# Kernel optimization log

Hardware: AMD Instinct MI355X
Metric: run time of the kernel (lower is better)

## Reference

```python
import jax, jax.numpy as jnp
import numpy as np
import math


def gen_slopes(n_heads, alibi_bias_max=1.0):
    # matches torch gen_slopes: _n_heads = next pow2, m = arange(1.._n)*max/_n, slopes = 2^-m
    _n = 2 ** math.ceil(math.log2(n_heads))
    m = jnp.arange(1, _n + 1, dtype=jnp.float32) * (alibi_bias_max / _n)
    slopes = 1.0 / jnp.power(2.0, m)
    if _n != n_heads:
        slopes = jnp.concatenate([slopes[1::2], slopes[::2]])[:n_heads]
    return slopes.reshape(1, n_heads, 1, 1)


def build_alibi_bias(n_heads, seq_len, alibi_bias_max=1.0):
    # full=False branch: bias over key positions only, shape [1, H, 1, L]
    pos = jnp.arange(1 - seq_len, 1, dtype=jnp.float32).reshape(1, 1, 1, seq_len)
    return pos * gen_slopes(n_heads, alibi_bias_max)


def setup_inputs() -> dict:
    key = jax.random.key(0)
    kq, kk, kv = jax.random.split(key, 3)
    B, L, H, E = 8, 1024, 8, 64
    return {
        "queries": jax.random.normal(kq, (B, L, H, E), dtype=jnp.float32),
        "keys": jax.random.normal(kk, (B, L, H, E), dtype=jnp.float32),
        "values": jax.random.normal(kv, (B, L, H, E), dtype=jnp.float32),
        "patch_index": -1,
    }


def reference(queries, keys, values, patch_index):
    B, L, H, E = queries.shape
    scale = 1.0 / math.sqrt(E)
    # scores: [B, H, L, L]
    scores = jnp.einsum('blhe,bshe->bhls', queries, keys)
    attn = scale * scores + build_alibi_bias(H, L)  # ALiBi bias, alibi_bias_max=1
    series = jax.nn.softmax(attn, axis=-1)  # dropout is identity in eval mode
    V = jnp.einsum('bhls,bshd->blhd', series, values)
    # patch_index == -1: identity branch, series unchanged
    return (V, series)
```

## Files before the change

### kernel.cpp

```cpp
#include <hip/hip_runtime.h>
#include <hip/hip_bf16.h>


typedef short short8 __attribute__((ext_vector_type(8)));
typedef short short4v __attribute__((ext_vector_type(4)));
typedef float f32x4 __attribute__((ext_vector_type(4)));
typedef unsigned short u16x4 __attribute__((ext_vector_type(4)));

#define B_ 8
#define L_ 1024
#define H_ 8
#define E_ 64
#define RSTRIDE (H_ * E_)
#define QBLK 64
#define CHUNK 128
#define NCH (L_ / CHUNK)
#define CHUNK_USH (CHUNK * E_)

__device__ __forceinline__ unsigned short f2bf(float f) {
  return __builtin_bit_cast(unsigned short, __float2bfloat16(f));
}
__device__ __forceinline__ short8 ldfrag(const float* p) {
  float4 a = *reinterpret_cast<const float4*>(p);
  float4 b = *reinterpret_cast<const float4*>(p + 4);
  return (short8){(short)f2bf(a.x), (short)f2bf(a.y), (short)f2bf(a.z),
                  (short)f2bf(a.w), (short)f2bf(b.x), (short)f2bf(b.y),
                  (short)f2bf(b.z), (short)f2bf(b.w)};
}

__device__ __forceinline__ f32x4 mfma16(short4v a, short4v b, f32x4 c) {
#if __has_builtin(__builtin_amdgcn_mfma_f32_16x16x16bf16_1k)
  return __builtin_amdgcn_mfma_f32_16x16x16bf16_1k(a, b, c, 0, 0, 0);
#else
  asm volatile(
      "s_nop 1\n\t"
      "v_mfma_f32_16x16x16_bf16 %0, %1, %2, %0\n\t"
      "s_nop 2"
      : "+v"(c)
      : "v"(a), "v"(b));
  return c;
#endif
}

__device__ __forceinline__ void gld16(const unsigned short* g,
                                      unsigned short* l) {
  __builtin_amdgcn_global_load_lds(
      (const __attribute__((address_space(1))) unsigned int*)g,
      (__attribute__((address_space(3))) unsigned int*)l, 16, 0, 0);
}

__global__ __launch_bounds__(256, 4) void prep_kv(
    const float* __restrict__ Kg, const float* __restrict__ Vg,
    unsigned short* __restrict__ Kbf, unsigned short* __restrict__ VTbf) {
  __shared__ unsigned short vt[64 * 128];

  const int t = threadIdx.x;
  const int id = blockIdx.x;
  const int bh = id & 63;
  const int sc = id >> 6;
  const int h = bh & 7, b = bh >> 3;
  const int s0 = sc * CHUNK;

  const float* Kb = Kg + ((size_t)b * L_ + s0) * RSTRIDE + h * E_;
  const float* Vb = Vg + ((size_t)b * L_ + s0) * RSTRIDE + h * E_;
  unsigned short* Ko = Kbf + (size_t)(bh * NCH + sc) * CHUNK_USH;
  unsigned short* Vo = VTbf + (size_t)(bh * NCH + sc) * CHUNK_USH;

#pragma unroll
  for (int i = 0; i < 4; ++i) {
    const int j = t + 256 * i;
    const int s = j >> 3;
    const int e8 = (j & 7) ^ (s & 7);
    const float* kp = Kb + (size_t)s * RSTRIDE + 8 * e8;
    float4 a = *reinterpret_cast<const float4*>(kp);
    float4 c = *reinterpret_cast<const float4*>(kp + 4);
    *reinterpret_cast<u16x4*>(&Ko[j * 8]) =
        (u16x4){f2bf(a.x), f2bf(a.y), f2bf(a.z), f2bf(a.w)};
    *reinterpret_cast<u16x4*>(&Ko[j * 8 + 4]) =
        (u16x4){f2bf(c.x), f2bf(c.y), f2bf(c.z), f2bf(c.w)};
  }
  {
    const int e = t & 63, w = t >> 6;
#pragma unroll
    for (int i = 0; i < 8; ++i) {
      const int s4 = 4 * w + 16 * i;
      const float* vp = Vb + (size_t)s4 * RSTRIDE + e;
      u16x4 u = {f2bf(vp[0]), f2bf(vp[RSTRIDE]), f2bf(vp[2 * RSTRIDE]),
                 f2bf(vp[3 * RSTRIDE])};
      *reinterpret_cast<u16x4*>(
          &vt[e * 128 + (((s4 >> 3) ^ (e & 7)) << 3) + (s4 & 7)]) = u;
    }
  }
  __syncthreads();
#pragma unroll
  for (int i = 0; i < 4; ++i) {
    const int j = t + 256 * i;
    u16x4 u0 = *reinterpret_cast<const u16x4*>(&vt[j * 8]);
    u16x4 u1 = *reinterpret_cast<const u16x4*>(&vt[j * 8 + 4]);
    *reinterpret_cast<u16x4*>(&Vo[j * 8]) = u0;
    *reinterpret_cast<u16x4*>(&Vo[j * 8 + 4]) = u1;
  }
}

__global__ __launch_bounds__(256, 4) void alibi_attn(
    const float* __restrict__ Qg, const unsigned short* __restrict__ Kbf,
    const unsigned short* __restrict__ VTbf, float* __restrict__ Vout,
    float* __restrict__ Pout) {
  __shared__ unsigned short sK[CHUNK_USH];
  __shared__ unsigned short sVT[CHUNK_USH];

  const int t = threadIdx.x;
  const int lane = t & 63;
  const int w = t >> 6;
  const int col = lane & 15;
  const int kg = lane >> 4;

  const int id = blockIdx.x;
  const int qb = id >> 6;
  const int bh = id & 63;
  const int h = bh & 7;
  const int b = bh >> 3;
  const int q0 = qb * QBLK;

  const float sc_l2e = 0.125f * 1.44269504f;
  const float sl_l2e = exp2f(-(float)(h + 1) * 0.125f) * 1.44269504f;

  const unsigned short* Kc = Kbf + (size_t)bh * NCH * CHUNK_USH;
  const unsigned short* Vc = VTbf + (size_t)bh * NCH * CHUNK_USH;

  short8 qf0, qf1;
  {
    const float* qp =
        Qg + ((size_t)b * L_ + q0 + 16 * w + col) * RSTRIDE + h * E_ + 8 * kg;
    qf0 = ldfrag(qp);
    qf1 = ldfrag(qp + 32);
  }

  const float kbias0 = sl_l2e * (float)(4 * kg - 1023) - 32.0f;

  float z0 = 0.f, z1 = 0.f, z2 = 0.f, z3 = 0.f;
  for (int c = 0; c < NCH; ++c) {
    {
      const unsigned short* src = Kc + (size_t)c * CHUNK_USH;
#pragma unroll
      for (int i = 0; i < 4; ++i) {
        const int seg = i * 4 + w;
        gld16(src + (size_t)(seg * 64 + lane) * 8, &sK[seg * 512]);
      }
    }
    __syncthreads();
#pragma unroll 4
    for (int kt = 0; kt < 8; ++kt) {
      const int row = 16 * kt + col;
      short8 k0 = *reinterpret_cast<const short8*>(
          &sK[row * 64 + ((kg ^ (row & 7)) << 3)]);
      short8 k1 = *reinterpret_cast<const short8*>(
          &sK[row * 64 + (((kg + 4) ^ (row & 7)) << 3)]);
      f32x4 acc = {0.f, 0.f, 0.f, 0.f};
      acc = __builtin_amdgcn_mfma_f32_16x16x32_bf16(k0, qf0, acc, 0, 0, 0);
      acc = __builtin_amdgcn_mfma_f32_16x16x32_bf16(k1, qf1, acc, 0, 0, 0);
      const float base = fmaf((float)(128 * c + 16 * kt), sl_l2e, kbias0);
      z0 += __builtin_amdgcn_exp2f(fmaf(acc[0], sc_l2e, base));
      z1 += __builtin_amdgcn_exp2f(fmaf(acc[1], sc_l2e, base + sl_l2e));
      z2 += __builtin_amdgcn_exp2f(fmaf(acc[2], sc_l2e, base + 2.f * sl_l2e));
      z3 += __builtin_amdgcn_exp2f(fmaf(acc[3], sc_l2e, base + 3.f * sl_l2e));
    }
    __syncthreads();
  }
  float z = (z0 + z1) + (z2 + z3);
  z += __shfl_xor(z, 16, 64);
  z += __shfl_xor(z, 32, 64);
  const float minv = 1.0f / z;

  f32x4 oacc[4];
#pragma unroll
  for (int et = 0; et < 4; ++et) oacc[et] = (f32x4){0.f, 0.f, 0.f, 0.f};

  float* Pb = Pout + ((size_t)(b * H_ + h) * L_ + q0 + 16 * w + col) * L_ +
              4 * kg;

  for (int c = 0; c < NCH; ++c) {
    {
      const unsigned short* srcK = Kc + (size_t)c * CHUNK_USH;
      const unsigned short* srcV = Vc + (size_t)c * CHUNK_USH;
#pragma unroll
      for (int i = 0; i < 4; ++i) {
        const int seg = i * 4 + w;
        gld16(srcK + (size_t)(seg * 64 + lane) * 8, &sK[seg * 512]);
        gld16(srcV + (size_t)(seg * 64 + lane) * 8, &sVT[seg * 512]);
      }
    }
    __syncthreads();
#pragma unroll 2
    for (int kt = 0; kt < 8; ++kt) {
      const int row = 16 * kt + col;
      short8 k0 = *reinterpret_cast<const short8*>(
          &sK[row * 64 + ((kg ^ (row & 7)) << 3)]);
      short8 k1 = *reinterpret_cast<const short8*>(
          &sK[row * 64 + (((kg + 4) ^ (row & 7)) << 3)]);
      f32x4 acc = {0.f, 0.f, 0.f, 0.f};
      acc = __builtin_amdgcn_mfma_f32_16x16x32_bf16(k0, qf0, acc, 0, 0, 0);
      acc = __builtin_amdgcn_mfma_f32_16x16x32_bf16(k1, qf1, acc, 0, 0, 0);
      short4v vf[4];
      const int g0 = 2 * kt + (kg >> 1);
      const int so = 4 * (kg & 1);
#pragma unroll
      for (int et = 0; et < 4; ++et) {
        const int e = 16 * et + col;
        vf[et] = *reinterpret_cast<const short4v*>(
            &sVT[e * 128 + ((g0 ^ (e & 7)) << 3) + so]);
      }
      const float base = fmaf((float)(128 * c + 16 * kt), sl_l2e, kbias0);
      f32x4 pf;
      pf[0] = __builtin_amdgcn_exp2f(fmaf(acc[0], sc_l2e, base)) * minv;
      pf[1] =
          __builtin_amdgcn_exp2f(fmaf(acc[1], sc_l2e, base + sl_l2e)) * minv;
      pf[2] = __builtin_amdgcn_exp2f(fmaf(acc[2], sc_l2e, base + 2.f * sl_l2e)) *
              minv;
      pf[3] = __builtin_amdgcn_exp2f(fmaf(acc[3], sc_l2e, base + 3.f * sl_l2e)) *
              minv;
      *reinterpret_cast<f32x4*>(Pb + 128 * c + 16 * kt) = pf;
      short4v pa = {(short)f2bf(pf[0]), (short)f2bf(pf[1]), (short)f2bf(pf[2]),
                    (short)f2bf(pf[3])};
#pragma unroll
      for (int et = 0; et < 4; ++et) oacc[et] = mfma16(pa, vf[et], oacc[et]);
    }
    __syncthreads();
  }

  float* Vo = Vout + (((size_t)b * L_ + q0 + 16 * w) * H_ + h) * E_;
#pragma unroll
  for (int et = 0; et < 4; ++et) {
#pragma unroll
    for (int r = 0; r < 4; ++r) {
      __builtin_nontemporal_store(oacc[et][r],
                                  &Vo[(4 * kg + r) * RSTRIDE + 16 * et + col]);
    }
  }
}

extern "C" void kernel_launch(void* const* d_in, const int* in_sizes, int n_in,
                              void* d_out, int out_size, void* d_ws,
                              size_t ws_size, hipStream_t stream) {
  const float* Q = (const float*)d_in[0];
  const float* K = (const float*)d_in[1];
  const float* V = (const float*)d_in[2];
  float* out = (float*)d_out;
  float* Vo = out;
  float* Po = out + (size_t)B_ * L_ * H_ * E_;
  unsigned short* Kbf = (unsigned short*)d_ws;
  unsigned short* VTbf = Kbf + (size_t)B_ * H_ * L_ * E_;
  hipLaunchKernelGGL(prep_kv, dim3(NCH * B_ * H_), dim3(256), 0, stream, K, V,
                     Kbf, VTbf);
  hipLaunchKernelGGL(alibi_attn, dim3((L_ / QBLK) * H_ * B_), dim3(256), 0,
                     stream, Q, Kbf, VTbf, Vo, Po);
}
```

Before: 95.58 us.

## Double-buffer K/V chunks in LDS and process two query tiles per wave

Each wave now handles 32 query rows (two 16-row tiles), so every K/V fragment read from LDS feeds twice the MFMA work. K and V chunks are halved to 64 keys and double-buffered in LDS, so the next chunk's global-to-LDS load overlaps compute on the current one and one barrier per chunk is dropped. The prep kernel is adjusted to the new chunk size. The cost is more registers and fewer blocks (launch bounds lowered to 2), which halves the grid to 512 blocks and reduces occupancy.

After: 121.7 us. 27.4% more time.

```diff
diff --git a/kernel.cpp b/kernel.cpp
--- a/kernel.cpp
+++ b/kernel.cpp
@@ -12,8 +12,8 @@
 #define H_ 8
 #define E_ 64
 #define RSTRIDE (H_ * E_)
-#define QBLK 64
-#define CHUNK 128
+#define QBLK 128
+#define CHUNK 64
 #define NCH (L_ / CHUNK)
 #define CHUNK_USH (CHUNK * E_)
 
@@ -52,7 +52,7 @@
 __global__ __launch_bounds__(256, 4) void prep_kv(
     const float* __restrict__ Kg, const float* __restrict__ Vg,
     unsigned short* __restrict__ Kbf, unsigned short* __restrict__ VTbf) {
-  __shared__ unsigned short vt[64 * 128];
+  __shared__ unsigned short vt[64 * 64];
 
   const int t = threadIdx.x;
   const int id = blockIdx.x;
@@ -67,7 +67,7 @@
   unsigned short* Vo = VTbf + (size_t)(bh * NCH + sc) * CHUNK_USH;
 
 #pragma unroll
-  for (int i = 0; i < 4; ++i) {
+  for (int i = 0; i < 2; ++i) {
     const int j = t + 256 * i;
     const int s = j >> 3;
     const int e8 = (j & 7) ^ (s & 7);
@@ -82,18 +82,18 @@
   {
     const int e = t & 63, w = t >> 6;
 #pragma unroll
-    for (int i = 0; i < 8; ++i) {
+    for (int i = 0; i < 4; ++i) {
       const int s4 = 4 * w + 16 * i;
       const float* vp = Vb + (size_t)s4 * RSTRIDE + e;
       u16x4 u = {f2bf(vp[0]), f2bf(vp[RSTRIDE]), f2bf(vp[2 * RSTRIDE]),
                  f2bf(vp[3 * RSTRIDE])};
       *reinterpret_cast<u16x4*>(
-          &vt[e * 128 + (((s4 >> 3) ^ (e & 7)) << 3) + (s4 & 7)]) = u;
+          &vt[e * 64 + (((s4 >> 3) ^ (e & 7)) << 3) + (s4 & 7)]) = u;
     }
   }
   __syncthreads();
 #pragma unroll
-  for (int i = 0; i < 4; ++i) {
+  for (int i = 0; i < 2; ++i) {
     const int j = t + 256 * i;
     u16x4 u0 = *reinterpret_cast<const u16x4*>(&vt[j * 8]);
     u16x4 u1 = *reinterpret_cast<const u16x4*>(&vt[j * 8 + 4]);
@@ -102,12 +102,12 @@
   }
 }
 
-__global__ __launch_bounds__(256, 4) void alibi_attn(
+__global__ __launch_bounds__(256, 2) void alibi_attn(
     const float* __restrict__ Qg, const unsigned short* __restrict__ Kbf,
     const unsigned short* __restrict__ VTbf, float* __restrict__ Vout,
     float* __restrict__ Pout) {
-  __shared__ unsigned short sK[CHUNK_USH];
-  __shared__ unsigned short sVT[CHUNK_USH];
+  __shared__ unsigned short sK[2][CHUNK_USH];
+  __shared__ unsigned short sVT[2][CHUNK_USH];
 
   const int t = threadIdx.x;
   const int lane = t & 63;
@@ -128,79 +128,103 @@
   const unsigned short* Kc = Kbf + (size_t)bh * NCH * CHUNK_USH;
   const unsigned short* Vc = VTbf + (size_t)bh * NCH * CHUNK_USH;
 
-  short8 qf0, qf1;
+  short8 qfA0, qfA1, qfB0, qfB1;
   {
     const float* qp =
-        Qg + ((size_t)b * L_ + q0 + 16 * w + col) * RSTRIDE + h * E_ + 8 * kg;
-    qf0 = ldfrag(qp);
-    qf1 = ldfrag(qp + 32);
+        Qg + ((size_t)b * L_ + q0 + 32 * w + col) * RSTRIDE + h * E_ + 8 * kg;
+    qfA0 = ldfrag(qp);
+    qfA1 = ldfrag(qp + 32);
+    qfB0 = ldfrag(qp + 16 * RSTRIDE);
+    qfB1 = ldfrag(qp + 16 * RSTRIDE + 32);
   }
 
   const float kbias0 = sl_l2e * (float)(4 * kg - 1023) - 32.0f;
 
-  float z0 = 0.f, z1 = 0.f, z2 = 0.f, z3 = 0.f;
+#define STAGE_K(c, bi)                                                    \
+  {                                                                       \
+    const unsigned short* src = Kc + (size_t)(c) * CHUNK_USH;             \
+    _Pragma("unroll") for (int i = 0; i < 2; ++i) {                       \
+      const int seg = i * 4 + w;                                          \
+      gld16(src + (size_t)(seg * 64 + lane) * 8, &sK[bi][seg * 512]);     \
+    }                                                                     \
+  }
+#define STAGE_V(c, bi)                                                    \
+  {                                                                       \
+    const unsigned short* src = Vc + (size_t)(c) * CHUNK_USH;             \
+    _Pragma("unroll") for (int i = 0; i < 2; ++i) {                       \
+      const int seg = i * 4 + w;                                          \
+      gld16(src + (size_t)(seg * 64 + lane) * 8, &sVT[bi][seg * 512]);    \
+    }                                                                     \
+  }
+
+  float zA = 0.f, zB = 0.f;
+  STAGE_K(0, 0);
+  __syncthreads();
   for (int c = 0; c < NCH; ++c) {
-    {
-      const unsigned short* src = Kc + (size_t)c * CHUNK_USH;
-#pragma unroll
-      for (int i = 0; i < 4; ++i) {
-        const int seg = i * 4 + w;
-        gld16(src + (size_t)(seg * 64 + lane) * 8, &sK[seg * 512]);
-      }
-    }
-    __syncthreads();
-#pragma unroll 4
-    for (int kt = 0; kt < 8; ++kt) {
+    if (c + 1 < NCH) STAGE_K(c + 1, (c + 1) & 1);
+    const unsigned short* kb = sK[c & 1];
+#pragma unroll
+    for (int kt = 0; kt < 4; ++kt) {
       const int row = 16 * kt + col;
       short8 k0 = *reinterpret_cast<const short8*>(
-          &sK[row * 64 + ((kg ^ (row & 7)) << 3)]);
+          &kb[row * 64 + ((kg ^ (row & 7)) << 3)]);
       short8 k1 = *reinterpret_cast<const short8*>(
-          &sK[row * 64 + (((kg + 4) ^ (row & 7)) << 3)]);
-      f32x4 acc = {0.f, 0.f, 0.f, 0.f};
-      acc = __builtin_amdgcn_mfma_f32_16x16x32_bf16(k0, qf0, acc, 0, 0, 0);
-      acc = __builtin_amdgcn_mfma_f32_16x16x32_bf16(k1, qf1, acc, 0, 0, 0);
-      const float base = fmaf((float)(128 * c + 16 * kt), sl_l2e, kbias0);
-      z0 += __builtin_amdgcn_exp2f(fmaf(acc[0], sc_l2e, base));
-      z1 += __builtin_amdgcn_exp2f(fmaf(acc[1], sc_l2e, base + sl_l2e));
-      z2 += __builtin_amdgcn_exp2f(fmaf(acc[2], sc_l2e, base + 2.f * sl_l2e));
-      z3 += __builtin_amdgcn_exp2f(fmaf(acc[3], sc_l2e, base + 3.f * sl_l2e));
+          &kb[row * 64 + (((kg + 4) ^ (row & 7)) << 3)]);
+      f32x4 aA = {0.f, 0.f, 0.f, 0.f}, aB = {0.f, 0.f, 0.f, 0.f};
+      aA = __builtin_amdgcn_mfma_f32_16x16x32_bf16(k0, qfA0, aA, 0, 0, 0);
+      aA = __builtin_amdgcn_mfma_f32_16x16x32_bf16(k1, qfA1, aA, 0, 0, 0);
+      aB = __builtin_amdgcn_mfma_f32_16x16x32_bf16(k0, qfB0, aB, 0, 0, 0);
+      aB = __builtin_amdgcn_mfma_f32_16x16x32_bf16(k1, qfB1, aB, 0, 0, 0);
+      const float base = fmaf((float)(CHUNK * c + 16 * kt), sl_l2e, kbias0);
+#pragma unroll
+      for (int r = 0; r < 4; ++r) {
+        const float bb = base + (float)r * sl_l2e;
+        zA += __builtin_amdgcn_exp2f(fmaf(aA[r], sc_l2e, bb));
+        zB += __builtin_amdgcn_exp2f(fmaf(aB[r], sc_l2e, bb));
+      }
     }
     __syncthreads();
   }
-  float z = (z0 + z1) + (z2 + z3);
-  z += __shfl_xor(z, 16, 64);
-  z += __shfl_xor(z, 32, 64);
-  const float minv = 1.0f / z;
-
-  f32x4 oacc[4];
-#pragma unroll
-  for (int et = 0; et < 4; ++et) oacc[et] = (f32x4){0.f, 0.f, 0.f, 0.f};
-
-  float* Pb = Pout + ((size_t)(b * H_ + h) * L_ + q0 + 16 * w + col) * L_ +
-              4 * kg;
-
+  zA += __shfl_xor(zA, 16, 64);
+  zA += __shfl_xor(zA, 32, 64);
+  zB += __shfl_xor(zB, 16, 64);
+  zB += __shfl_xor(zB, 32, 64);
+  const float minvA = 1.0f / zA;
+  const float minvB = 1.0f / zB;
+
+  f32x4 oA[4], oB[4];
+#pragma unroll
+  for (int et = 0; et < 4; ++et) {
+    oA[et] = (f32x4){0.f, 0.f, 0.f, 0.f};
+    oB[et] = (f32x4){0.f, 0.f, 0.f, 0.f};
+  }
+
+  float* PbA = Pout + ((size_t)(b * H_ + h) * L_ + q0 + 32 * w + col) * L_ +
+               4 * kg;
+  float* PbB = PbA + (size_t)16 * L_;
+
+  STAGE_K(0, 0);
+  STAGE_V(0, 0);
+  __syncthreads();
   for (int c = 0; c < NCH; ++c) {
-    {
-      const unsigned short* srcK = Kc + (size_t)c * CHUNK_USH;
-      const unsigned short* srcV = Vc + (size_t)c * CHUNK_USH;
-#pragma unroll
-      for (int i = 0; i < 4; ++i) {
-        const int seg = i * 4 + w;
-        gld16(srcK + (size_t)(seg * 64 + lane) * 8, &sK[seg * 512]);
-        gld16(srcV + (size_t)(seg * 64 + lane) * 8, &sVT[seg * 512]);
-      }
-    }
-    __syncthreads();
-#pragma unroll 2
-    for (int kt = 0; kt < 8; ++kt) {
+    if (c + 1 < NCH) {
+      STAGE_K(c + 1, (c + 1) & 1);
+      STAGE_V(c + 1, (c + 1) & 1);
+    }
+    const unsigned short* kb = sK[c & 1];
+    const unsigned short* vb = sVT[c & 1];
+#pragma unroll
+    for (int kt = 0; kt < 4; ++kt) {
       const int row = 16 * kt + col;
       short8 k0 = *reinterpret_cast<const short8*>(
-          &sK[row * 64 + ((kg ^ (row & 7)) << 3)]);
+          &kb[row * 64 + ((kg ^ (row & 7)) << 3)]);
       short8 k1 = *reinterpret_cast<const short8*>(
-          &sK[row * 64 + (((kg + 4) ^ (row & 7)) << 3)]);
-      f32x4 acc = {0.f, 0.f, 0.f, 0.f};
-      acc = __builtin_amdgcn_mfma_f32_16x16x32_bf16(k0, qf0, acc, 0, 0, 0);
-      acc = __builtin_amdgcn_mfma_f32_16x16x32_bf16(k1, qf1, acc, 0, 0, 0);
+          &kb[row * 64 + (((kg + 4) ^ (row & 7)) << 3)]);
+      f32x4 aA = {0.f, 0.f, 0.f, 0.f}, aB = {0.f, 0.f, 0.f, 0.f};
+      aA = __builtin_amdgcn_mfma_f32_16x16x32_bf16(k0, qfA0, aA, 0, 0, 0);
+      aA = __builtin_amdgcn_mfma_f32_16x16x32_bf16(k1, qfA1, aA, 0, 0, 0);
+      aB = __builtin_amdgcn_mfma_f32_16x16x32_bf16(k0, qfB0, aB, 0, 0, 0);
+      aB = __builtin_amdgcn_mfma_f32_16x16x32_bf16(k1, qfB1, aB, 0, 0, 0);
       short4v vf[4];
       const int g0 = 2 * kt + (kg >> 1);
       const int so = 4 * (kg & 1);
@@ -208,33 +232,41 @@
       for (int et = 0; et < 4; ++et) {
         const int e = 16 * et + col;
         vf[et] = *reinterpret_cast<const short4v*>(
-            &sVT[e * 128 + ((g0 ^ (e & 7)) << 3) + so]);
-      }
-      const float base = fmaf((float)(128 * c + 16 * kt), sl_l2e, kbias0);
-      f32x4 pf;
-      pf[0] = __builtin_amdgcn_exp2f(fmaf(acc[0], sc_l2e, base)) * minv;
-      pf[1] =
-          __builtin_amdgcn_exp2f(fmaf(acc[1], sc_l2e, base + sl_l2e)) * minv;
-      pf[2] = __builtin_amdgcn_exp2f(fmaf(acc[2], sc_l2e, base + 2.f * sl_l2e)) *
-              minv;
-      pf[3] = __builtin_amdgcn_exp2f(fmaf(acc[3], sc_l2e, base + 3.f * sl_l2e)) *
-              minv;
-      *reinterpret_cast<f32x4*>(Pb + 128 * c + 16 * kt) = pf;
-      short4v pa = {(short)f2bf(pf[0]), (short)f2bf(pf[1]), (short)f2bf(pf[2]),
-                    (short)f2bf(pf[3])};
-#pragma unroll
-      for (int et = 0; et < 4; ++et) oacc[et] = mfma16(pa, vf[et], oacc[et]);
+            &vb[e * 64 + ((g0 ^ (e & 7)) << 3) + so]);
+      }
+      const float base = fmaf((float)(CHUNK * c + 16 * kt), sl_l2e, kbias0);
+      f32x4 pA, pB;
+#pragma unroll
+      for (int r = 0; r < 4; ++r) {
+        const float bb = base + (float)r * sl_l2e;
+        pA[r] = __builtin_amdgcn_exp2f(fmaf(aA[r], sc_l2e, bb)) * minvA;
+        pB[r] = __builtin_amdgcn_exp2f(fmaf(aB[r], sc_l2e, bb)) * minvB;
+      }
+      *reinterpret_cast<f32x4*>(PbA + CHUNK * c + 16 * kt) = pA;
+      *reinterpret_cast<f32x4*>(PbB + CHUNK * c + 16 * kt) = pB;
+      short4v paA = {(short)f2bf(pA[0]), (short)f2bf(pA[1]),
+                     (short)f2bf(pA[2]), (short)f2bf(pA[3])};
+      short4v paB = {(short)f2bf(pB[0]), (short)f2bf(pB[1]),
+                     (short)f2bf(pB[2]), (short)f2bf(pB[3])};
+#pragma unroll
+      for (int et = 0; et < 4; ++et) {
+        oA[et] = mfma16(paA, vf[et], oA[et]);
+        oB[et] = mfma16(paB, vf[et], oB[et]);
+      }
     }
     __syncthreads();
   }
 
-  float* Vo = Vout + (((size_t)b * L_ + q0 + 16 * w) * H_ + h) * E_;
+  float* VoA = Vout + (((size_t)b * L_ + q0 + 32 * w) * H_ + h) * E_;
+  float* VoB = VoA + (size_t)16 * RSTRIDE;
 #pragma unroll
   for (int et = 0; et < 4; ++et) {
 #pragma unroll
     for (int r = 0; r < 4; ++r) {
-      __builtin_nontemporal_store(oacc[et][r],
-                                  &Vo[(4 * kg + r) * RSTRIDE + 16 * et + col]);
+      __builtin_nontemporal_store(oA[et][r],
+                                  &VoA[(4 * kg + r) * RSTRIDE + 16 * et + col]);
+      __builtin_nontemporal_store(oB[et][r],
+                                  &VoB[(4 * kg + r) * RSTRIDE + 16 * et + col]);
     }
   }
 }
```

## Double-buffer K/V LDS staging with smaller 64-key chunks

Applied to the files above, without the earlier changes.

Halves the key chunk size from 128 to 64 and double-buffers the K and V^T shared-memory tiles. The next chunk's async global-to-LDS load is issued before computing on the current one, so the load can overlap with the MFMA and exp work, and one barrier per chunk is removed. The prep kernel is resized to match the new chunk layout. Total LDS use stays the same, but the number of chunk iterations and barriers doubles. The kernel may also be limited mostly by the large fp32 probability write, which would cap any gain.

New measurement: 105.5 us. 1.1x slower.

```diff
diff --git a/kernel.cpp b/kernel.cpp
--- a/kernel.cpp
+++ b/kernel.cpp
@@ -13,7 +13,7 @@
 #define E_ 64
 #define RSTRIDE (H_ * E_)
 #define QBLK 64
-#define CHUNK 128
+#define CHUNK 64
 #define NCH (L_ / CHUNK)
 #define CHUNK_USH (CHUNK * E_)
 
@@ -52,7 +52,7 @@
 __global__ __launch_bounds__(256, 4) void prep_kv(
     const float* __restrict__ Kg, const float* __restrict__ Vg,
     unsigned short* __restrict__ Kbf, unsigned short* __restrict__ VTbf) {
-  __shared__ unsigned short vt[64 * 128];
+  __shared__ unsigned short vt[64 * 64];
 
   const int t = threadIdx.x;
   const int id = blockIdx.x;
@@ -67,7 +67,7 @@
   unsigned short* Vo = VTbf + (size_t)(bh * NCH + sc) * CHUNK_USH;
 
 #pragma unroll
-  for (int i = 0; i < 4; ++i) {
+  for (int i = 0; i < 2; ++i) {
     const int j = t + 256 * i;
     const int s = j >> 3;
     const int e8 = (j & 7) ^ (s & 7);
@@ -82,18 +82,18 @@
   {
     const int e = t & 63, w = t >> 6;
 #pragma unroll
-    for (int i = 0; i < 8; ++i) {
+    for (int i = 0; i < 4; ++i) {
       const int s4 = 4 * w + 16 * i;
       const float* vp = Vb + (size_t)s4 * RSTRIDE + e;
       u16x4 u = {f2bf(vp[0]), f2bf(vp[RSTRIDE]), f2bf(vp[2 * RSTRIDE]),
                  f2bf(vp[3 * RSTRIDE])};
       *reinterpret_cast<u16x4*>(
-          &vt[e * 128 + (((s4 >> 3) ^ (e & 7)) << 3) + (s4 & 7)]) = u;
+          &vt[e * 64 + (((s4 >> 3) ^ (e & 7)) << 3) + (s4 & 7)]) = u;
     }
   }
   __syncthreads();
 #pragma unroll
-  for (int i = 0; i < 4; ++i) {
+  for (int i = 0; i < 2; ++i) {
     const int j = t + 256 * i;
     u16x4 u0 = *reinterpret_cast<const u16x4*>(&vt[j * 8]);
     u16x4 u1 = *reinterpret_cast<const u16x4*>(&vt[j * 8 + 4]);
@@ -106,8 +106,8 @@
     const float* __restrict__ Qg, const unsigned short* __restrict__ Kbf,
     const unsigned short* __restrict__ VTbf, float* __restrict__ Vout,
     float* __restrict__ Pout) {
-  __shared__ unsigned short sK[CHUNK_USH];
-  __shared__ unsigned short sVT[CHUNK_USH];
+  __shared__ unsigned short sK[2][CHUNK_USH];
+  __shared__ unsigned short sVT[2][CHUNK_USH];
 
   const int t = threadIdx.x;
   const int lane = t & 63;
@@ -138,28 +138,40 @@
 
   const float kbias0 = sl_l2e * (float)(4 * kg - 1023) - 32.0f;
 
+#define STAGE_K(c, bi)                                                  \
+  {                                                                     \
+    const unsigned short* src = Kc + (size_t)(c) * CHUNK_USH;           \
+    _Pragma("unroll") for (int i = 0; i < 2; ++i) {                     \
+      const int seg = i * 4 + w;                                        \
+      gld16(src + (size_t)(seg * 64 + lane) * 8, &sK[bi][seg * 512]);   \
+    }                                                                   \
+  }
+#define STAGE_V(c, bi)                                                  \
+  {                                                                     \
+    const unsigned short* src = Vc + (size_t)(c) * CHUNK_USH;           \
+    _Pragma("unroll") for (int i = 0; i < 2; ++i) {                     \
+      const int seg = i * 4 + w;                                        \
+      gld16(src + (size_t)(seg * 64 + lane) * 8, &sVT[bi][seg * 512]);  \
+    }                                                                   \
+  }
+
   float z0 = 0.f, z1 = 0.f, z2 = 0.f, z3 = 0.f;
+  STAGE_K(0, 0);
+  __syncthreads();
   for (int c = 0; c < NCH; ++c) {
-    {
-      const unsigned short* src = Kc + (size_t)c * CHUNK_USH;
-#pragma unroll
-      for (int i = 0; i < 4; ++i) {
-        const int seg = i * 4 + w;
-        gld16(src + (size_t)(seg * 64 + lane) * 8, &sK[seg * 512]);
-      }
-    }
-    __syncthreads();
-#pragma unroll 4
-    for (int kt = 0; kt < 8; ++kt) {
+    if (c + 1 < NCH) STAGE_K(c + 1, (c + 1) & 1);
+    const unsigned short* kb = sK[c & 1];
+#pragma unroll
+    for (int kt = 0; kt < 4; ++kt) {
       const int row = 16 * kt + col;
       short8 k0 = *reinterpret_cast<const short8*>(
-          &sK[row * 64 + ((kg ^ (row & 7)) << 3)]);
+          &kb[row * 64 + ((kg ^ (row & 7)) << 3)]);
       short8 k1 = *reinterpret_cast<const short8*>(
-          &sK[row * 64 + (((kg + 4) ^ (row & 7)) << 3)]);
+          &kb[row * 64 + (((kg + 4) ^ (row & 7)) << 3)]);
       f32x4 acc = {0.f, 0.f, 0.f, 0.f};
       acc = __builtin_amdgcn_mfma_f32_16x16x32_bf16(k0, qf0, acc, 0, 0, 0);
       acc = __builtin_amdgcn_mfma_f32_16x16x32_bf16(k1, qf1, acc, 0, 0, 0);
-      const float base = fmaf((float)(128 * c + 16 * kt), sl_l2e, kbias0);
+      const float base = fmaf((float)(CHUNK * c + 16 * kt), sl_l2e, kbias0);
       z0 += __builtin_amdgcn_exp2f(fmaf(acc[0], sc_l2e, base));
       z1 += __builtin_amdgcn_exp2f(fmaf(acc[1], sc_l2e, base + sl_l2e));
       z2 += __builtin_amdgcn_exp2f(fmaf(acc[2], sc_l2e, base + 2.f * sl_l2e));
@@ -176,28 +188,26 @@
 #pragma unroll
   for (int et = 0; et < 4; ++et) oacc[et] = (f32x4){0.f, 0.f, 0.f, 0.f};
 
-  float* Pb = Pout + ((size_t)(b * H_ + h) * L_ + q0 + 16 * w + col) * L_ +
-              4 * kg;
-
+  float* Pb =
+      Pout + ((size_t)(b * H_ + h) * L_ + q0 + 16 * w + col) * L_ + 4 * kg;
+
+  STAGE_K(0, 0);
+  STAGE_V(0, 0);
+  __syncthreads();
   for (int c = 0; c < NCH; ++c) {
-    {
-      const unsigned short* srcK = Kc + (size_t)c * CHUNK_USH;
-      const unsigned short* srcV = Vc + (size_t)c * CHUNK_USH;
-#pragma unroll
-      for (int i = 0; i < 4; ++i) {
-        const int seg = i * 4 + w;
-        gld16(srcK + (size_t)(seg * 64 + lane) * 8, &sK[seg * 512]);
-        gld16(srcV + (size_t)(seg * 64 + lane) * 8, &sVT[seg * 512]);
-      }
-    }
-    __syncthreads();
-#pragma unroll 2
-    for (int kt = 0; kt < 8; ++kt) {
+    if (c + 1 < NCH) {
+      STAGE_K(c + 1, (c + 1) & 1);
+      STAGE_V(c + 1, (c + 1) & 1);
+    }
+    const unsigned short* kb = sK[c & 1];
+    const unsigned short* vb = sVT[c & 1];
+#pragma unroll
+    for (int kt = 0; kt < 4; ++kt) {
       const int row = 16 * kt + col;
       short8 k0 = *reinterpret_cast<const short8*>(
-          &sK[row * 64 + ((kg ^ (row & 7)) << 3)]);
+          &kb[row * 64 + ((kg ^ (row & 7)) << 3)]);
       short8 k1 = *reinterpret_cast<const short8*>(
-          &sK[row * 64 + (((kg + 4) ^ (row & 7)) << 3)]);
+          &kb[row * 64 + (((kg + 4) ^ (row & 7)) << 3)]);
       f32x4 acc = {0.f, 0.f, 0.f, 0.f};
       acc = __builtin_amdgcn_mfma_f32_16x16x32_bf16(k0, qf0, acc, 0, 0, 0);
       acc = __builtin_amdgcn_mfma_f32_16x16x32_bf16(k1, qf1, acc, 0, 0, 0);
@@ -208,9 +218,9 @@
       for (int et = 0; et < 4; ++et) {
         const int e = 16 * et + col;
         vf[et] = *reinterpret_cast<const short4v*>(
-            &sVT[e * 128 + ((g0 ^ (e & 7)) << 3) + so]);
+            &vb[e * 64 + ((g0 ^ (e & 7)) << 3) + so]);
       }
-      const float base = fmaf((float)(128 * c + 16 * kt), sl_l2e, kbias0);
+      const float base = fmaf((float)(CHUNK * c + 16 * kt), sl_l2e, kbias0);
       f32x4 pf;
       pf[0] = __builtin_amdgcn_exp2f(fmaf(acc[0], sc_l2e, base)) * minv;
       pf[1] =
@@ -219,7 +229,7 @@
               minv;
       pf[3] = __builtin_amdgcn_exp2f(fmaf(acc[3], sc_l2e, base + 3.f * sl_l2e)) *
               minv;
-      *reinterpret_cast<f32x4*>(Pb + 128 * c + 16 * kt) = pf;
+      *reinterpret_cast<f32x4*>(Pb + CHUNK * c + 16 * kt) = pf;
       short4v pa = {(short)f2bf(pf[0]), (short)f2bf(pf[1]), (short)f2bf(pf[2]),
                     (short)f2bf(pf[3])};
 #pragma unroll
```
